# Performance work log

Hardware: AMD Instinct MI355X
Metric: run time of the kernel (lower is better)

Reference implementation:

```python
import jax, jax.numpy as jnp
import numpy as np

TOP_K = 2
INIT_STD = 0.02
B, T, D, E, I = 2, 2048, 1024, 8, 512


def setup_inputs() -> dict:
    key = jax.random.key(0)
    k0, k1, k2, k3, k4 = jax.random.split(key, 5)
    return {
        "x": jax.random.normal(k0, (B, T, D), dtype=jnp.float32),
        "router_w": (jax.random.normal(k1, (E, D), dtype=jnp.float32) * INIT_STD),
        "w_gate": (jax.random.normal(k2, (E, I, D), dtype=jnp.float32) * INIT_STD),
        "w_up": (jax.random.normal(k3, (E, I, D), dtype=jnp.float32) * INIT_STD),
        "w_down": (jax.random.normal(k4, (E, D, I), dtype=jnp.float32) * INIT_STD),
    }


def _moe_forward(x, router_w, w_gate, w_up, w_down):
    # x: [B, T, D]; router_w: [E, D]; w_gate/w_up: [E, I, D]; w_down: [E, D, I]
    b, t, d = x.shape
    e = router_w.shape[0]
    gate_logits = jnp.einsum('btd,ed->bte', x, router_w)          # [B, T, E]
    top_w, sel = jax.lax.top_k(gate_logits, TOP_K)                # [B, T, K]
    probs = jax.nn.softmax(top_w, axis=-1)                        # softmax over selected experts only

    n = b * t
    xf = x.reshape(n, d)                                          # [N, D]
    sel_f = sel.reshape(n, TOP_K)
    probs_f = probs.reshape(n, TOP_K)
    # combine weights per (token, expert); zero for unselected experts
    gates = jnp.zeros((n, e), dtype=x.dtype).at[
        jnp.arange(n)[:, None], sel_f].add(probs_f)               # [N, E]

    # SwiGLU expert FFN (no bias). Gated-dense formulation: unselected experts
    # have gate weight exactly 0, so this is bit-for-bit the same math as
    # dispatch + grouped GEMM + combine. scan over experts keeps memory at
    # one [N, I] intermediate at a time.
    def body(acc, ws):
        wg, wu, wd, g = ws                                        # [I,D],[I,D],[D,I],[N]
        h = jax.nn.silu(xf @ wg.T) * (xf @ wu.T)                  # [N, I]
        return acc + g[:, None] * (h @ wd.T), None

    out, _ = jax.lax.scan(body, jnp.zeros((n, d), dtype=x.dtype),
                          (w_gate, w_up, w_down, gates.T))
    return out.reshape(b, t, d), gate_logits


def reference(x, router_w, w_gate, w_up, w_down):
    return _moe_forward(x, router_w, w_gate, w_up, w_down)
```

## Files before the change

### kernel.cpp

```cpp
#include <hip/hip_runtime.h>
#include <cstdint>

#define N_TOK 4096
#define D_    1024
#define E_    8
#define I_    512
#define PAD   64
#define CAP   (N_TOK*2 + E_*PAD)
#define NBX   (CAP / PAD)
#define WSZ   ((size_t)E_ * I_ * D_)

typedef __attribute__((ext_vector_type(16))) float f32x16;
typedef __attribute__((ext_vector_type(8)))  short bf16x8;

__device__ inline unsigned short f2bf(float f) {
  union { float f; uint32_t u; } v; v.f = f;
  uint32_t r = v.u + 0x7fffu + ((v.u >> 16) & 1u);
  return (unsigned short)(r >> 16);
}
__device__ inline float bf2f(unsigned short h) {
  union { uint32_t u; float f; } v; v.u = ((uint32_t)h) << 16;
  return v.f;
}

#define GLOAD_LDS16(gp, lp)                                                        \
  __builtin_amdgcn_global_load_lds((const __attribute__((address_space(1))) void*)(gp), \
                                   (__attribute__((address_space(3))) void*)(lp), 16, 0, 0)

__global__ __launch_bounds__(256) void prep_kernel(const float* __restrict__ x,
                                                   const float* __restrict__ rw,
                                                   const float* __restrict__ wg,
                                                   const float* __restrict__ wu,
                                                   const float* __restrict__ wd,
                                                   float* __restrict__ logits,
                                                   int* __restrict__ sel,
                                                   float* __restrict__ prob,
                                                   unsigned short* __restrict__ Xb,
                                                   unsigned short* __restrict__ Wb) {
  int b = blockIdx.x;
  if (b < 3 * 4096) {
    const int y = b >> 12;
    const float* s = (y == 0) ? wg : (y == 1) ? wu : wd;
    unsigned short* d = Wb + (size_t)y * WSZ;
    const int i = (b & 4095) * 256 + threadIdx.x;
    const float4 v = reinterpret_cast<const float4*>(s)[i];
    ushort4 o;
    o.x = f2bf(v.x); o.y = f2bf(v.y); o.z = f2bf(v.z); o.w = f2bf(v.w);
    reinterpret_cast<ushort4*>(d)[i] = o;
    return;
  }
  b -= 3 * 4096;
  const int lane = threadIdx.x & 63;
  const int tok  = b * 4 + (threadIdx.x >> 6);
  const float4* xr = reinterpret_cast<const float4*>(x + (size_t)tok * D_);
  float4 xv[4];
#pragma unroll
  for (int q = 0; q < 4; ++q) xv[q] = xr[q * 64 + lane];
  float acc[E_];
#pragma unroll
  for (int e = 0; e < E_; ++e) {
    const float4* wr = reinterpret_cast<const float4*>(rw + (size_t)e * D_);
    float s = 0.f;
#pragma unroll
    for (int q = 0; q < 4; ++q) {
      float4 wv = wr[q * 64 + lane];
      s += xv[q].x * wv.x + xv[q].y * wv.y + xv[q].z * wv.z + xv[q].w * wv.w;
    }
    acc[e] = s;
  }
  ushort4* xb = reinterpret_cast<ushort4*>(Xb + (size_t)tok * D_);
#pragma unroll
  for (int q = 0; q < 4; ++q) {
    ushort4 o;
    o.x = f2bf(xv[q].x); o.y = f2bf(xv[q].y); o.z = f2bf(xv[q].z); o.w = f2bf(xv[q].w);
    xb[q * 64 + lane] = o;
  }
#pragma unroll
  for (int e = 0; e < E_; ++e)
#pragma unroll
    for (int off = 32; off; off >>= 1) acc[e] += __shfl_xor(acc[e], off);
  if (lane == 0) {
    float v0 = -1e30f, v1 = -1e30f; int i0 = 0, i1 = 0;
#pragma unroll
    for (int e = 0; e < E_; ++e) {
      float v = acc[e];
      logits[(size_t)tok * E_ + e] = v;
      if (v > v0)      { v1 = v0; i1 = i0; v0 = v; i0 = e; }
      else if (v > v1) { v1 = v;  i1 = e; }
    }
    float t  = __expf(v1 - v0);
    sel[tok * 2] = i0; sel[tok * 2 + 1] = i1;
    prob[tok * 2] = 1.f / (1.f + t);
    prob[tok * 2 + 1] = t / (1.f + t);
  }
}

__global__ __launch_bounds__(1024) void plan_kernel(const int* __restrict__ sel,
                                                    const float* __restrict__ prob,
                                                    int* __restrict__ offs,
                                                    int* __restrict__ ptok,
                                                    float* __restrict__ pprob,
                                                    int* __restrict__ tpos) {
  __shared__ int wcnt[16][E_];
  __shared__ int pfx[16][E_];
  __shared__ int soffs[E_ + 1];
  __shared__ int secnt[E_];
  const int tid = threadIdx.x;
  const int wave = tid >> 6, lane = tid & 63;
  const unsigned long long lt = (1ull << lane) - 1ull;

  int   mye[8];
  int   mylp[8];
  float myp[8];
  int run[E_];
#pragma unroll
  for (int e = 0; e < E_; ++e) run[e] = 0;

#pragma unroll
  for (int it = 0; it < 8; ++it) {
    int i = wave * 512 + it * 64 + lane;
    int e = sel[i];
    mye[it] = e;
    myp[it] = prob[i];
    int lp = 0;
#pragma unroll
    for (int ee = 0; ee < E_; ++ee) {
      unsigned long long m = __ballot(e == ee);
      if (e == ee) lp = run[ee] + __popcll(m & lt);
      run[ee] += __popcll(m);
    }
    mylp[it] = lp;
  }
#pragma unroll
  for (int ee = 0; ee < E_; ++ee)
    if (lane == ee) wcnt[wave][ee] = run[ee];
  __syncthreads();

  if (tid == 0) {
    int ro = 0;
#pragma unroll
    for (int e = 0; e < E_; ++e) {
      int c = 0;
      int r = ro;
      for (int w = 0; w < 16; ++w) { pfx[w][e] = r; r += wcnt[w][e]; c += wcnt[w][e]; }
      soffs[e] = ro; offs[e] = ro; secnt[e] = c;
      ro += (c + PAD - 1) & ~(PAD - 1);
    }
    soffs[E_] = ro; offs[E_] = ro;
  }
  __syncthreads();

#pragma unroll
  for (int it = 0; it < 8; ++it) {
    int i = wave * 512 + it * 64 + lane;
    int pos = pfx[wave][mye[it]] + mylp[it];
    ptok[pos]  = i >> 1;
    pprob[pos] = myp[it];
    tpos[i]    = pos;
  }
#pragma unroll
  for (int e = 0; e < E_; ++e) {
    int s = soffs[e] + secnt[e];
    int npad = soffs[e + 1] - s;
    if (tid < npad) { ptok[s + tid] = 0; pprob[s + tid] = 0.f; }
  }
}

__global__ __launch_bounds__(256, 3) void gemm1_kernel(const unsigned short* __restrict__ Xb,
                                                       const unsigned short* __restrict__ Wg,
                                                       const unsigned short* __restrict__ Wu,
                                                       const int* __restrict__ ptok,
                                                       const int* __restrict__ offs,
                                                       unsigned short* __restrict__ H) {
  __shared__ unsigned short As[PAD * 128];
  __shared__ unsigned short Bg[64 * 128];
  __shared__ unsigned short Bu[64 * 128];
  __shared__ int toks[PAD];

  const int wgid = (blockIdx.x & 7) * 136 + (blockIdx.x >> 3);
  const int bx = wgid >> 3;
  const int by = wgid & 7;

  const int total = offs[E_];
  const int t0 = bx * PAD;
  if (t0 >= total) return;
  int e = 0;
#pragma unroll
  for (int i = 1; i < E_; ++i) if (offs[i] <= t0) e = i;

  const int tid  = threadIdx.x;
  const int lane = tid & 63;
  const int w    = tid >> 6;
  if (tid < PAD) toks[tid] = ptok[t0 + tid];
  __syncthreads();

  const int ib = by * 64;

  const unsigned short* asrc[4];
  const unsigned short* bgsrc[4];
  const unsigned short* busrc[4];
#pragma unroll
  for (int i = 0; i < 4; ++i) {
    const int r  = w * 16 + i * 4 + (lane >> 4);
    const int gc = (lane & 15) ^ (r & 15);
    asrc[i] = Xb + (size_t)toks[r] * D_ + gc * 8;
    const size_t rowoff = ((size_t)e * I_ + ib + r) * D_ + gc * 8;
    bgsrc[i] = Wg + rowoff;
    busrc[i] = Wu + rowoff;
  }

  f32x16 accg, accu;
#pragma unroll
  for (int j = 0; j < 16; ++j) { accg[j] = 0.f; accu[j] = 0.f; }

  const int wr = w >> 1, wc = w & 1;
  const int xr15 = lane & 15;
  const int arow = wr * 32 + (lane & 31);
  const int brow = wc * 32 + (lane & 31);

  for (int k0 = 0; k0 < D_; k0 += 128) {
#pragma unroll
    for (int i = 0; i < 4; ++i) {
      GLOAD_LDS16(asrc[i] + k0, &As[(w * 4 + i) * 512]);
      GLOAD_LDS16(bgsrc[i] + k0, &Bg[(w * 4 + i) * 512]);
      GLOAD_LDS16(busrc[i] + k0, &Bu[(w * 4 + i) * 512]);
    }
    __syncthreads();
#pragma unroll
    for (int sk = 0; sk < 8; ++sk) {
      const int uoff = ((sk * 2 + (lane >> 5)) ^ xr15) * 8;
      bf16x8 a  = *reinterpret_cast<const bf16x8*>(&As[arow * 128 + uoff]);
      bf16x8 bg = *reinterpret_cast<const bf16x8*>(&Bg[brow * 128 + uoff]);
      bf16x8 bu = *reinterpret_cast<const bf16x8*>(&Bu[brow * 128 + uoff]);
      accg = __builtin_amdgcn_mfma_f32_32x32x16_bf16(bg, a, accg, 0, 0, 0);
      accu = __builtin_amdgcn_mfma_f32_32x32x16_bf16(bu, a, accu, 0, 0, 0);
    }
    __syncthreads();
  }

  const int hrow = t0 + wr * 32 + (lane & 31);
#pragma unroll
  for (int q = 0; q < 4; ++q) {
    const int icb = ib + wc * 32 + q * 8 + (lane >> 5) * 4;
    ushort4 st;
    float g, uu, h;
    g = accg[q*4+0]; uu = accu[q*4+0]; h = (g / (1.f + __expf(-g))) * uu; st.x = f2bf(h);
    g = accg[q*4+1]; uu = accu[q*4+1]; h = (g / (1.f + __expf(-g))) * uu; st.y = f2bf(h);
    g = accg[q*4+2]; uu = accu[q*4+2]; h = (g / (1.f + __expf(-g))) * uu; st.z = f2bf(h);
    g = accg[q*4+3]; uu = accu[q*4+3]; h = (g / (1.f + __expf(-g))) * uu; st.w = f2bf(h);
    *reinterpret_cast<ushort4*>(&H[(size_t)hrow * I_ + icb]) = st;
  }
}

__global__ __launch_bounds__(256, 4) void gemm2_kernel(const unsigned short* __restrict__ H,
                                                       const unsigned short* __restrict__ Wd,
                                                       const float* __restrict__ pprob,
                                                       const int* __restrict__ offs,
                                                       unsigned short* __restrict__ O) {
  __shared__ unsigned short As[PAD * 64];
  __shared__ unsigned short Bs[128 * 64];
  __shared__ float probs[PAD];

  const int wgid = (blockIdx.x & 7) * 136 + (blockIdx.x >> 3);
  const int bx = wgid >> 3;
  const int by = wgid & 7;

  const int total = offs[E_];
  const int t0 = bx * PAD;
  if (t0 >= total) return;
  int e = 0;
#pragma unroll
  for (int i = 1; i < E_; ++i) if (offs[i] <= t0) e = i;

  const int tid  = threadIdx.x;
  const int lane = tid & 63;
  const int w    = tid >> 6;
  if (tid < PAD) probs[tid] = pprob[t0 + tid];
  __syncthreads();

  const int db    = by * 128;
  const int gcol8 = (lane & 7) ^ (lane >> 3);

  const unsigned short* asrc[2];
#pragma unroll
  for (int i = 0; i < 2; ++i) {
    int r = w * 16 + i * 8 + (lane >> 3);
    asrc[i] = H + (size_t)(t0 + r) * I_ + gcol8 * 8;
  }
  const unsigned short* bsrc[4];
#pragma unroll
  for (int i = 0; i < 4; ++i) {
    int r = w * 32 + i * 8 + (lane >> 3);
    bsrc[i] = Wd + ((size_t)e * D_ + db + r) * I_ + gcol8 * 8;
  }

  f32x16 acc0, acc1;
#pragma unroll
  for (int j = 0; j < 16; ++j) { acc0[j] = 0.f; acc1[j] = 0.f; }

  const int wr = w >> 1, wc = w & 1;
  const int xr7 = lane & 7;
  const int arow  = wr * 32 + (lane & 31);
  const int brow0 = wc * 64 + (lane & 31);
  const int brow1 = wc * 64 + 32 + (lane & 31);

  for (int k0 = 0; k0 < I_; k0 += 64) {
#pragma unroll
    for (int i = 0; i < 2; ++i) GLOAD_LDS16(asrc[i] + k0, &As[(w * 2 + i) * 512]);
#pragma unroll
    for (int i = 0; i < 4; ++i) GLOAD_LDS16(bsrc[i] + k0, &Bs[(w * 4 + i) * 512]);
    __syncthreads();
#pragma unroll
    for (int sk = 0; sk < 4; ++sk) {
      const int uoff = ((sk * 2 + (lane >> 5)) ^ xr7) * 8;
      bf16x8 a  = *reinterpret_cast<const bf16x8*>(&As[arow * 64 + uoff]);
      bf16x8 b0 = *reinterpret_cast<const bf16x8*>(&Bs[brow0 * 64 + uoff]);
      bf16x8 b1 = *reinterpret_cast<const bf16x8*>(&Bs[brow1 * 64 + uoff]);
      acc0 = __builtin_amdgcn_mfma_f32_32x32x16_bf16(b0, a, acc0, 0, 0, 0);
      acc1 = __builtin_amdgcn_mfma_f32_32x32x16_bf16(b1, a, acc1, 0, 0, 0);
    }
    __syncthreads();
  }

  const int prow = wr * 32 + (lane & 31);
  const float p = probs[prow];
  const int orow = t0 + prow;
#pragma unroll
  for (int q = 0; q < 4; ++q) {
    const int dcb0 = db + wc * 64 + q * 8 + (lane >> 5) * 4;
    ushort4 v;
    v.x = f2bf(acc0[q*4+0] * p); v.y = f2bf(acc0[q*4+1] * p);
    v.z = f2bf(acc0[q*4+2] * p); v.w = f2bf(acc0[q*4+3] * p);
    *reinterpret_cast<ushort4*>(&O[(size_t)orow * D_ + dcb0]) = v;
    ushort4 v1;
    v1.x = f2bf(acc1[q*4+0] * p); v1.y = f2bf(acc1[q*4+1] * p);
    v1.z = f2bf(acc1[q*4+2] * p); v1.w = f2bf(acc1[q*4+3] * p);
    *reinterpret_cast<ushort4*>(&O[(size_t)orow * D_ + dcb0 + 32]) = v1;
  }
}

__global__ __launch_bounds__(256) void combine_kernel(const unsigned short* __restrict__ O,
                                                      const int* __restrict__ tpos,
                                                      float* __restrict__ out) {
  const int t = blockIdx.x;
  const int c = threadIdx.x;
  const int p0 = tpos[2 * t], p1 = tpos[2 * t + 1];
  const ushort4 a = reinterpret_cast<const ushort4*>(O + (size_t)p0 * D_)[c];
  const ushort4 b = reinterpret_cast<const ushort4*>(O + (size_t)p1 * D_)[c];
  float4 r;
  r.x = bf2f(a.x) + bf2f(b.x); r.y = bf2f(a.y) + bf2f(b.y);
  r.z = bf2f(a.z) + bf2f(b.z); r.w = bf2f(a.w) + bf2f(b.w);
  reinterpret_cast<float4*>(out + (size_t)t * D_)[c] = r;
}

extern "C" void kernel_launch(void* const* d_in, const int* in_sizes, int n_in,
                              void* d_out, int out_size, void* d_ws, size_t ws_size,
                              hipStream_t stream) {
  const float* x  = (const float*)d_in[0];
  const float* rw = (const float*)d_in[1];
  const float* wg = (const float*)d_in[2];
  const float* wu = (const float*)d_in[3];
  const float* wd = (const float*)d_in[4];
  float* out    = (float*)d_out;
  float* logits = out + (size_t)N_TOK * D_;

  char* ws = (char*)d_ws;
  int*   offs  = (int*)  (ws + 64);
  int*   sel   = (int*)  (ws + 4352);
  float* prob  = (float*)(ws + 37120);
  int*   ptok  = (int*)  (ws + 69888);
  float* pprob = (float*)(ws + 104704);
  int*   tpos  = (int*)  (ws + 139520);
  unsigned short* Xb  = (unsigned short*)(ws + 172288);
  unsigned short* Wgb = Xb  + (size_t)N_TOK * D_;
  unsigned short* Wub = Wgb + WSZ;
  unsigned short* Wdb = Wub + WSZ;
  unsigned short* Hb  = Wdb + WSZ;
  unsigned short* Opos = Hb + (size_t)CAP * I_;

  prep_kernel<<<3 * 4096 + N_TOK / 4, 256, 0, stream>>>(x, rw, wg, wu, wd,
                                                        logits, sel, prob, Xb, Wgb);
  plan_kernel<<<1, 1024, 0, stream>>>(sel, prob, offs, ptok, pprob, tpos);
  gemm1_kernel<<<NBX * 8, 256, 0, stream>>>(Xb, Wgb, Wub, ptok, offs, Hb);
  gemm2_kernel<<<NBX * 8, 256, 0, stream>>>(Hb, Wdb, pprob, offs, Opos);
  combine_kernel<<<N_TOK, 256, 0, stream>>>(Opos, tpos, out);
}
```

Baseline: 92.19 us.

## Use per-wave private LDS tiles and move w_down conversion into gemm1

Each wave in both grouped GEMMs now loads its own A/B sub-tiles into a private LDS slice, so block-wide __syncthreads are replaced by a per-wave vmcnt wait and sched barriers. The cost being targeted is barrier stalls between waves. In exchange, A/B data that used to be shared across waves is now loaded redundantly. The w_down fp32-to-bf16 conversion moves out of prep_kernel into extra trailing blocks of gemm1, so it can overlap with the GEMM work instead of lengthening prep. gemm2 occupancy hints drop from 4 to 3 and its K-loop load pattern changes.

```diff
diff --git a/kernel.cpp b/kernel.cpp
--- a/kernel.cpp
+++ b/kernel.cpp
@@ -7,7 +7,7 @@
 #define I_    512
 #define PAD   64
 #define CAP   (N_TOK*2 + E_*PAD)
-#define NBX   (CAP / PAD)
+#define NBT   1088
 #define WSZ   ((size_t)E_ * I_ * D_)
 
 typedef __attribute__((ext_vector_type(16))) float f32x16;
@@ -27,20 +27,25 @@
   __builtin_amdgcn_global_load_lds((const __attribute__((address_space(1))) void*)(gp), \
                                    (__attribute__((address_space(3))) void*)(lp), 16, 0, 0)
 
+#define WAVE_FENCE                                       \
+  do {                                                   \
+    asm volatile("s_waitcnt vmcnt(0)" ::: "memory");     \
+    __builtin_amdgcn_sched_barrier(0);                   \
+  } while (0)
+
 __global__ __launch_bounds__(256) void prep_kernel(const float* __restrict__ x,
                                                    const float* __restrict__ rw,
                                                    const float* __restrict__ wg,
                                                    const float* __restrict__ wu,
-                                                   const float* __restrict__ wd,
                                                    float* __restrict__ logits,
                                                    int* __restrict__ sel,
                                                    float* __restrict__ prob,
                                                    unsigned short* __restrict__ Xb,
                                                    unsigned short* __restrict__ Wb) {
   int b = blockIdx.x;
-  if (b < 3 * 4096) {
+  if (b < 2 * 4096) {
     const int y = b >> 12;
-    const float* s = (y == 0) ? wg : (y == 1) ? wu : wd;
+    const float* s = (y == 0) ? wg : wu;
     unsigned short* d = Wb + (size_t)y * WSZ;
     const int i = (b & 4095) * 256 + threadIdx.x;
     const float4 v = reinterpret_cast<const float4*>(s)[i];
@@ -49,7 +54,7 @@
     reinterpret_cast<ushort4*>(d)[i] = o;
     return;
   }
-  b -= 3 * 4096;
+  b -= 2 * 4096;
   const int lane = threadIdx.x & 63;
   const int tok  = b * 4 + (threadIdx.x >> 6);
   const float4* xr = reinterpret_cast<const float4*>(x + (size_t)tok * D_);
@@ -169,79 +174,91 @@
 __global__ __launch_bounds__(256, 3) void gemm1_kernel(const unsigned short* __restrict__ Xb,
                                                        const unsigned short* __restrict__ Wg,
                                                        const unsigned short* __restrict__ Wu,
+                                                       const float* __restrict__ wd,
                                                        const int* __restrict__ ptok,
                                                        const int* __restrict__ offs,
+                                                       unsigned short* __restrict__ Wdb,
                                                        unsigned short* __restrict__ H) {
-  __shared__ unsigned short As[PAD * 128];
-  __shared__ unsigned short Bg[64 * 128];
-  __shared__ unsigned short Bu[64 * 128];
-  __shared__ int toks[PAD];
-
-  const int wgid = (blockIdx.x & 7) * 136 + (blockIdx.x >> 3);
+  __shared__ unsigned short lds[4][3][2048];
+  const int bid = blockIdx.x;
+  const int tid = threadIdx.x;
+  const int lane = tid & 63;
+  const int w    = tid >> 6;
+
+  if (bid >= NBT) {
+    const int base = (bid - NBT) * 256 + tid;
+#pragma unroll
+    for (int it = 0; it < 4; ++it) {
+      const int idx = base + it * 1024 * 256;
+      const float4 v = reinterpret_cast<const float4*>(wd)[idx];
+      ushort4 o;
+      o.x = f2bf(v.x); o.y = f2bf(v.y); o.z = f2bf(v.z); o.w = f2bf(v.w);
+      reinterpret_cast<ushort4*>(Wdb)[idx] = o;
+    }
+    return;
+  }
+
+  const int wgid = (bid & 7) * 136 + (bid >> 3);
   const int bx = wgid >> 3;
   const int by = wgid & 7;
-
   const int total = offs[E_];
-  const int t0 = bx * PAD;
+  const int t0 = bx * 64;
   if (t0 >= total) return;
   int e = 0;
 #pragma unroll
   for (int i = 1; i < E_; ++i) if (offs[i] <= t0) e = i;
 
-  const int tid  = threadIdx.x;
-  const int lane = tid & 63;
-  const int w    = tid >> 6;
-  if (tid < PAD) toks[tid] = ptok[t0 + tid];
-  __syncthreads();
-
-  const int ib = by * 64;
+  const int wr = w >> 1, wc = w & 1;
+  const int wt0 = t0 + wr * 32;
+  const int ic0 = by * 64 + wc * 32;
+  const int gc8 = ((lane & 7) ^ (lane >> 3)) * 8;
 
   const unsigned short* asrc[4];
   const unsigned short* bgsrc[4];
   const unsigned short* busrc[4];
 #pragma unroll
-  for (int i = 0; i < 4; ++i) {
-    const int r  = w * 16 + i * 4 + (lane >> 4);
-    const int gc = (lane & 15) ^ (r & 15);
-    asrc[i] = Xb + (size_t)toks[r] * D_ + gc * 8;
-    const size_t rowoff = ((size_t)e * I_ + ib + r) * D_ + gc * 8;
-    bgsrc[i] = Wg + rowoff;
-    busrc[i] = Wu + rowoff;
-  }
+  for (int j = 0; j < 4; ++j) {
+    const int r = j * 8 + (lane >> 3);
+    asrc[j] = Xb + (size_t)ptok[wt0 + r] * D_ + gc8;
+    const size_t ro = ((size_t)e * I_ + ic0 + r) * D_ + gc8;
+    bgsrc[j] = Wg + ro;
+    busrc[j] = Wu + ro;
+  }
+
+  unsigned short* A  = lds[w][0];
+  unsigned short* Bg = lds[w][1];
+  unsigned short* Bu = lds[w][2];
 
   f32x16 accg, accu;
 #pragma unroll
   for (int j = 0; j < 16; ++j) { accg[j] = 0.f; accu[j] = 0.f; }
 
-  const int wr = w >> 1, wc = w & 1;
-  const int xr15 = lane & 15;
-  const int arow = wr * 32 + (lane & 31);
-  const int brow = wc * 32 + (lane & 31);
-
-  for (int k0 = 0; k0 < D_; k0 += 128) {
-#pragma unroll
-    for (int i = 0; i < 4; ++i) {
-      GLOAD_LDS16(asrc[i] + k0, &As[(w * 4 + i) * 512]);
-      GLOAD_LDS16(bgsrc[i] + k0, &Bg[(w * 4 + i) * 512]);
-      GLOAD_LDS16(busrc[i] + k0, &Bu[(w * 4 + i) * 512]);
-    }
-    __syncthreads();
-#pragma unroll
-    for (int sk = 0; sk < 8; ++sk) {
-      const int uoff = ((sk * 2 + (lane >> 5)) ^ xr15) * 8;
-      bf16x8 a  = *reinterpret_cast<const bf16x8*>(&As[arow * 128 + uoff]);
-      bf16x8 bg = *reinterpret_cast<const bf16x8*>(&Bg[brow * 128 + uoff]);
-      bf16x8 bu = *reinterpret_cast<const bf16x8*>(&Bu[brow * 128 + uoff]);
+  const int arow64 = (lane & 31) * 64;
+
+  for (int k0 = 0; k0 < D_; k0 += 64) {
+#pragma unroll
+    for (int j = 0; j < 4; ++j) {
+      GLOAD_LDS16(asrc[j] + k0, &A[j * 512]);
+      GLOAD_LDS16(bgsrc[j] + k0, &Bg[j * 512]);
+      GLOAD_LDS16(busrc[j] + k0, &Bu[j * 512]);
+    }
+    WAVE_FENCE;
+#pragma unroll
+    for (int sk = 0; sk < 4; ++sk) {
+      const int uoff = ((sk * 2 + (lane >> 5)) ^ (lane & 7)) * 8;
+      bf16x8 a  = *reinterpret_cast<const bf16x8*>(&A[arow64 + uoff]);
+      bf16x8 bg = *reinterpret_cast<const bf16x8*>(&Bg[arow64 + uoff]);
+      bf16x8 bu = *reinterpret_cast<const bf16x8*>(&Bu[arow64 + uoff]);
       accg = __builtin_amdgcn_mfma_f32_32x32x16_bf16(bg, a, accg, 0, 0, 0);
       accu = __builtin_amdgcn_mfma_f32_32x32x16_bf16(bu, a, accu, 0, 0, 0);
     }
-    __syncthreads();
-  }
-
-  const int hrow = t0 + wr * 32 + (lane & 31);
+    __builtin_amdgcn_sched_barrier(0);
+  }
+
+  const int hrow = wt0 + (lane & 31);
 #pragma unroll
   for (int q = 0; q < 4; ++q) {
-    const int icb = ib + wc * 32 + q * 8 + (lane >> 5) * 4;
+    const int icb = ic0 + q * 8 + (lane >> 5) * 4;
     ushort4 st;
     float g, uu, h;
     g = accg[q*4+0]; uu = accu[q*4+0]; h = (g / (1.f + __expf(-g))) * uu; st.x = f2bf(h);
@@ -252,90 +269,85 @@
   }
 }
 
-__global__ __launch_bounds__(256, 4) void gemm2_kernel(const unsigned short* __restrict__ H,
+__global__ __launch_bounds__(256, 3) void gemm2_kernel(const unsigned short* __restrict__ H,
                                                        const unsigned short* __restrict__ Wd,
                                                        const float* __restrict__ pprob,
                                                        const int* __restrict__ offs,
                                                        unsigned short* __restrict__ O) {
-  __shared__ unsigned short As[PAD * 64];
-  __shared__ unsigned short Bs[128 * 64];
-  __shared__ float probs[PAD];
-
-  const int wgid = (blockIdx.x & 7) * 136 + (blockIdx.x >> 3);
+  __shared__ unsigned short lds[4][6144];
+  const int bid = blockIdx.x;
+  const int tid = threadIdx.x;
+  const int lane = tid & 63;
+  const int w    = tid >> 6;
+
+  const int wgid = (bid & 7) * 136 + (bid >> 3);
   const int bx = wgid >> 3;
   const int by = wgid & 7;
-
   const int total = offs[E_];
-  const int t0 = bx * PAD;
+  const int t0 = bx * 64;
   if (t0 >= total) return;
   int e = 0;
 #pragma unroll
   for (int i = 1; i < E_; ++i) if (offs[i] <= t0) e = i;
 
-  const int tid  = threadIdx.x;
-  const int lane = tid & 63;
-  const int w    = tid >> 6;
-  if (tid < PAD) probs[tid] = pprob[t0 + tid];
-  __syncthreads();
-
-  const int db    = by * 128;
-  const int gcol8 = (lane & 7) ^ (lane >> 3);
-
-  const unsigned short* asrc[2];
-#pragma unroll
-  for (int i = 0; i < 2; ++i) {
-    int r = w * 16 + i * 8 + (lane >> 3);
-    asrc[i] = H + (size_t)(t0 + r) * I_ + gcol8 * 8;
-  }
-  const unsigned short* bsrc[4];
-#pragma unroll
-  for (int i = 0; i < 4; ++i) {
-    int r = w * 32 + i * 8 + (lane >> 3);
-    bsrc[i] = Wd + ((size_t)e * D_ + db + r) * I_ + gcol8 * 8;
+  const int wr = w >> 1, wc = w & 1;
+  const int wt0 = t0 + wr * 32;
+  const int dc0 = by * 128 + wc * 64;
+  const int gc8 = ((lane & 7) ^ (lane >> 3)) * 8;
+
+  unsigned short* A = &lds[w][0];
+  unsigned short* B = A + 2048;
+
+  const unsigned short* asrc[4];
+#pragma unroll
+  for (int j = 0; j < 4; ++j) {
+    const int r = j * 8 + (lane >> 3);
+    asrc[j] = H + (size_t)(wt0 + r) * I_ + gc8;
+  }
+  const unsigned short* bsrc[8];
+#pragma unroll
+  for (int j = 0; j < 8; ++j) {
+    const int r = j * 8 + (lane >> 3);
+    bsrc[j] = Wd + ((size_t)e * D_ + dc0 + r) * I_ + gc8;
   }
 
   f32x16 acc0, acc1;
 #pragma unroll
   for (int j = 0; j < 16; ++j) { acc0[j] = 0.f; acc1[j] = 0.f; }
 
-  const int wr = w >> 1, wc = w & 1;
-  const int xr7 = lane & 7;
-  const int arow  = wr * 32 + (lane & 31);
-  const int brow0 = wc * 64 + (lane & 31);
-  const int brow1 = wc * 64 + 32 + (lane & 31);
+  const int arow64 = (lane & 31) * 64;
 
   for (int k0 = 0; k0 < I_; k0 += 64) {
 #pragma unroll
-    for (int i = 0; i < 2; ++i) GLOAD_LDS16(asrc[i] + k0, &As[(w * 2 + i) * 512]);
-#pragma unroll
-    for (int i = 0; i < 4; ++i) GLOAD_LDS16(bsrc[i] + k0, &Bs[(w * 4 + i) * 512]);
-    __syncthreads();
+    for (int j = 0; j < 4; ++j) GLOAD_LDS16(asrc[j] + k0, &A[j * 512]);
+#pragma unroll
+    for (int j = 0; j < 8; ++j) GLOAD_LDS16(bsrc[j] + k0, &B[j * 512]);
+    WAVE_FENCE;
 #pragma unroll
     for (int sk = 0; sk < 4; ++sk) {
-      const int uoff = ((sk * 2 + (lane >> 5)) ^ xr7) * 8;
-      bf16x8 a  = *reinterpret_cast<const bf16x8*>(&As[arow * 64 + uoff]);
-      bf16x8 b0 = *reinterpret_cast<const bf16x8*>(&Bs[brow0 * 64 + uoff]);
-      bf16x8 b1 = *reinterpret_cast<const bf16x8*>(&Bs[brow1 * 64 + uoff]);
+      const int uoff = ((sk * 2 + (lane >> 5)) ^ (lane & 7)) * 8;
+      bf16x8 a  = *reinterpret_cast<const bf16x8*>(&A[arow64 + uoff]);
+      bf16x8 b0 = *reinterpret_cast<const bf16x8*>(&B[arow64 + uoff]);
+      bf16x8 b1 = *reinterpret_cast<const bf16x8*>(&B[2048 + arow64 + uoff]);
       acc0 = __builtin_amdgcn_mfma_f32_32x32x16_bf16(b0, a, acc0, 0, 0, 0);
       acc1 = __builtin_amdgcn_mfma_f32_32x32x16_bf16(b1, a, acc1, 0, 0, 0);
     }
-    __syncthreads();
-  }
-
-  const int prow = wr * 32 + (lane & 31);
-  const float p = probs[prow];
-  const int orow = t0 + prow;
+    __builtin_amdgcn_sched_barrier(0);
+  }
+
+  const float p = pprob[wt0 + (lane & 31)];
+  const int orow = wt0 + (lane & 31);
 #pragma unroll
   for (int q = 0; q < 4; ++q) {
-    const int dcb0 = db + wc * 64 + q * 8 + (lane >> 5) * 4;
+    const int dcb = dc0 + q * 8 + (lane >> 5) * 4;
     ushort4 v;
     v.x = f2bf(acc0[q*4+0] * p); v.y = f2bf(acc0[q*4+1] * p);
     v.z = f2bf(acc0[q*4+2] * p); v.w = f2bf(acc0[q*4+3] * p);
-    *reinterpret_cast<ushort4*>(&O[(size_t)orow * D_ + dcb0]) = v;
+    *reinterpret_cast<ushort4*>(&O[(size_t)orow * D_ + dcb]) = v;
     ushort4 v1;
     v1.x = f2bf(acc1[q*4+0] * p); v1.y = f2bf(acc1[q*4+1] * p);
     v1.z = f2bf(acc1[q*4+2] * p); v1.w = f2bf(acc1[q*4+3] * p);
-    *reinterpret_cast<ushort4*>(&O[(size_t)orow * D_ + dcb0 + 32]) = v1;
+    *reinterpret_cast<ushort4*>(&O[(size_t)orow * D_ + dcb + 32]) = v1;
   }
 }
 
@@ -378,10 +390,10 @@
   unsigned short* Hb  = Wdb + WSZ;
   unsigned short* Opos = Hb + (size_t)CAP * I_;
 
-  prep_kernel<<<3 * 4096 + N_TOK / 4, 256, 0, stream>>>(x, rw, wg, wu, wd,
+  prep_kernel<<<2 * 4096 + N_TOK / 4, 256, 0, stream>>>(x, rw, wg, wu,
                                                         logits, sel, prob, Xb, Wgb);
   plan_kernel<<<1, 1024, 0, stream>>>(sel, prob, offs, ptok, pprob, tpos);
-  gemm1_kernel<<<NBX * 8, 256, 0, stream>>>(Xb, Wgb, Wub, ptok, offs, Hb);
-  gemm2_kernel<<<NBX * 8, 256, 0, stream>>>(Hb, Wdb, pprob, offs, Opos);
+  gemm1_kernel<<<NBT + 1024, 256, 0, stream>>>(Xb, Wgb, Wub, wd, ptok, offs, Wdb, Hb);
+  gemm2_kernel<<<NBT, 256, 0, stream>>>(Hb, Wdb, pprob, offs, Opos);
   combine_kernel<<<N_TOK, 256, 0, stream>>>(Opos, tpos, out);
 }
```

Result: slower. 104.3 us (+13.2%).
